# Kernel tuning notes

Hardware: AMD Instinct MI355X
Metric: run time of the kernel (lower is better)

Reference implementation:

```python
import jax, jax.numpy as jnp
import numpy as np

EPS = 1e-5


def _layer_norm(x, gamma, beta):
    mu = jnp.mean(x, axis=-1, keepdims=True)
    var = jnp.var(x, axis=-1, keepdims=True)
    return (x - mu) * jax.lax.rsqrt(var + EPS) * gamma + beta


def setup_inputs() -> dict:
    key = jax.random.key(0)
    B, I, H = 4096, 1024, 1024
    ks = jax.random.split(key, 6)
    x = jax.random.normal(ks[0], (B, I), dtype=jnp.float32)
    h = jax.random.normal(ks[1], (B, H), dtype=jnp.float32)
    c = jax.random.normal(ks[2], (B, H), dtype=jnp.float32)
    # nn.Linear(I+H, 4H): weight [4H, I+H], bias [4H]
    bound = 1.0 / np.sqrt(I + H)
    W = jax.random.uniform(ks[3], (4 * H, I + H), minval=-bound, maxval=bound, dtype=jnp.float32)
    b = jax.random.uniform(ks[4], (4 * H,), minval=-bound, maxval=bound, dtype=jnp.float32)
    inp = {"x": x, "h": h, "c": c, "W": W, "b": b}
    for name in ("i", "f", "g", "o", "c"):
        inp[f"ln_{name}_g"] = jnp.ones((H,), dtype=jnp.float32)
        inp[f"ln_{name}_b"] = jnp.zeros((H,), dtype=jnp.float32)
    return inp


def reference(x, h, c, W, b, ln_i_g, ln_i_b, ln_f_g, ln_f_b, ln_g_g, ln_g_b,
              ln_o_g, ln_o_b, ln_c_g, ln_c_b):
    H = h.shape[-1]
    xh = jnp.concatenate([x, h], axis=-1)              # [B, I+H]
    gates = xh @ W.T + b                               # [B, 4H]
    i_raw, f_raw, g_raw, o_raw = jnp.split(gates, 4, axis=-1)
    i = jax.nn.sigmoid(_layer_norm(i_raw, ln_i_g, ln_i_b))
    f = jax.nn.sigmoid(_layer_norm(f_raw, ln_f_g, ln_f_b))
    g = jnp.tanh(_layer_norm(g_raw, ln_g_g, ln_g_b))
    o = jax.nn.sigmoid(_layer_norm(o_raw, ln_o_g, ln_o_b))
    c_new = f * c + i * g
    h_new = o * jnp.tanh(_layer_norm(c_new, ln_c_g, ln_c_b))
    return (h_new, c_new)
```

## Files before the change

kernel.cpp:

```cpp
#include <hip/hip_runtime.h>
#include <hip/hip_bf16.h>

#define B_ROWS 4096
#define H_DIM  1024
#define K_DIM  2048
#define N_DIM  4096
#define NT32   64

typedef __attribute__((ext_vector_type(8))) short bf16x8;
typedef __attribute__((ext_vector_type(4))) float f32x4;

__device__ __forceinline__ unsigned short f2bf(float f) {
  union { float f; unsigned int u; } v; v.f = f;
  unsigned int u = v.u;
  return (unsigned short)((u + 0x7fffu + ((u >> 16) & 1u)) >> 16);
}
__device__ __forceinline__ float bf2f(unsigned short u) {
  union { unsigned int u; float f; } v; v.u = ((unsigned int)u) << 16;
  return v.f;
}

__device__ __forceinline__ void gload_lds16(const void* g, void* l) {
  __builtin_amdgcn_global_load_lds(
      (const __attribute__((address_space(1))) void*)g,
      (__attribute__((address_space(3))) void*)l, 16, 0, 0);
}

__global__ __launch_bounds__(256) void pack_kernel(
    const float* __restrict__ x, const float* __restrict__ h,
    const float* __restrict__ W, unsigned short* __restrict__ Abf,
    unsigned short* __restrict__ Wbf) {
  int bid = blockIdx.x;
  if (bid < 8192) {
    int t = bid * 256 + threadIdx.x;
    int e = t * 4;
    int row = e >> 11;
    int col = e & 2047;
    const float* src = (col < 1024) ? (x + (size_t)row * 1024 + col)
                                    : (h + (size_t)row * 1024 + (col - 1024));
    float4 v = *(const float4*)src;
    ushort4 o;
    o.x = f2bf(v.x); o.y = f2bf(v.y); o.z = f2bf(v.z); o.w = f2bf(v.w);
    *(ushort4*)(Abf + e) = o;
  } else {
    int t = (bid - 8192) * 256 + threadIdx.x;
    int e = t * 4;
    float4 v = *(const float4*)(W + e);
    ushort4 o;
    o.x = f2bf(v.x); o.y = f2bf(v.y); o.z = f2bf(v.z); o.w = f2bf(v.w);
    *(ushort4*)(Wbf + e) = o;
  }
}


#define UNR _Pragma("unroll")

#define TILE1(tt, BUF, FRa, FRb, FWa, FWb)                                   \
  {                                                                          \
    const int kt3 = ((tt) + 3) & (NT32 - 1);                                 \
    char* const Ld = lds + (((BUF) + 3) & 3) * 32768;                        \
    const unsigned short* pA = gAw + ((size_t)kt3 << 5);                     \
    const unsigned short* pB = gBw + ((size_t)kt3 << 5);                     \
    gload_lds16(pA, Ld + dstOfs);                                            \
    gload_lds16(pA + 16 * K_DIM, Ld + dstOfs + 1024);                        \
    gload_lds16(pB, Ld + 16384 + dstOfs);                                    \
    gload_lds16(pB + 16 * K_DIM, Ld + 16384 + dstOfs + 1024);                \
    asm volatile("s_waitcnt vmcnt(8)" ::: "memory");                         \
    __builtin_amdgcn_s_barrier();                                            \
    const char* const Ln = lds + (((BUF) + 1) & 3) * 32768;                  \
    UNR for (int mi = 0; mi < 8; ++mi)                                       \
      FWa[mi] = *(const bf16x8*)(Ln + (wm * 8 + mi) * 1024 + lofs);          \
    UNR for (int ni = 0; ni < 4; ++ni)                                       \
      FWb[ni] = *(const bf16x8*)(Ln + 16384 + (wn * 4 + ni) * 1024 + lofs);  \
    asm volatile("s_waitcnt lgkmcnt(12)" ::: "memory");                      \
    __builtin_amdgcn_sched_barrier(0);                                       \
    __builtin_amdgcn_s_setprio(1);                                           \
    UNR for (int mi = 0; mi < 8; ++mi)                                       \
      UNR for (int ni = 0; ni < 4; ++ni)                                     \
        acc[mi][ni] = __builtin_amdgcn_mfma_f32_16x16x32_bf16(               \
            FRa[mi], FRb[ni], acc[mi][ni], 0, 0, 0);                         \
    __builtin_amdgcn_s_setprio(0);                                           \
  }

#define PSTAGE(kt, BUFOFS)                                                   \
  {                                                                          \
    const unsigned short* pA = gAw + ((size_t)(kt) << 5);                    \
    const unsigned short* pB = gBw + ((size_t)(kt) << 5);                    \
    char* const Ld = lds + (BUFOFS);                                         \
    gload_lds16(pA, Ld + dstOfs);                                            \
    gload_lds16(pA + 16 * K_DIM, Ld + dstOfs + 1024);                        \
    gload_lds16(pB, Ld + 16384 + dstOfs);                                    \
    gload_lds16(pB + 16 * K_DIM, Ld + 16384 + dstOfs + 1024);                \
  }

__global__ __launch_bounds__(512, 2) void gemm_kernel(
    const unsigned short* __restrict__ A, const unsigned short* __restrict__ W,
    const float* __restrict__ bias, unsigned short* __restrict__ C) {
  __shared__ __align__(16) char lds[131072];

  const int tid = threadIdx.x;
  const int w = tid >> 6, l = tid & 63;
  const int wm = w >> 2, wn = w & 3;

  const int bid = blockIdx.x;
  const int xcd = bid & 7, li = bid >> 3;
  const int by = (xcd & 3) * 4 + (li >> 3);
  const int bx = ((xcd >> 2) << 3) + (li & 7);
  const int bm = by * 256, bn = bx * 256;

  const int lofs = (((l & 15) * 64) + ((l >> 4) * 16)) ^ ((l & 8) << 2);
  const int lane_r = (l >> 2) & 15;
  const int lane_c = ((l & 3) * 8) ^ (((l >> 5) & 1) * 16);

  const int dstOfs = w * 2048;
  const unsigned short* gAw = A + (size_t)(bm + 32 * w + lane_r) * K_DIM + lane_c;
  const unsigned short* gBw = W + (size_t)(bn + 32 * w + lane_r) * K_DIM + lane_c;

  f32x4 acc[8][4];
#pragma unroll
  for (int i = 0; i < 8; ++i)
#pragma unroll
    for (int j = 0; j < 4; ++j) acc[i][j] = (f32x4)0.0f;

  PSTAGE(0, 0);
  PSTAGE(1, 32768);
  PSTAGE(2, 65536);
  asm volatile("s_waitcnt vmcnt(8)" ::: "memory");
  __builtin_amdgcn_s_barrier();

  bf16x8 aP[8], bP[4], aQ[8], bQ[4];
#pragma unroll
  for (int mi = 0; mi < 8; ++mi)
    aP[mi] = *(const bf16x8*)(lds + (wm * 8 + mi) * 1024 + lofs);
#pragma unroll
  for (int ni = 0; ni < 4; ++ni)
    bP[ni] = *(const bf16x8*)(lds + 16384 + (wn * 4 + ni) * 1024 + lofs);

  for (int t = 0; t < NT32; t += 4) {
    TILE1(t + 0, 0, aP, bP, aQ, bQ);
    TILE1(t + 1, 1, aQ, bQ, aP, bP);
    TILE1(t + 2, 2, aP, bP, aQ, bQ);
    TILE1(t + 3, 3, aQ, bQ, aP, bP);
  }

  const int lm = l & 15, lq = l >> 4;
  float bv[4];
#pragma unroll
  for (int ni = 0; ni < 4; ++ni) bv[ni] = bias[bn + wn * 64 + ni * 16 + lm];
  unsigned short* Cb = C + (size_t)(bm + wm * 128) * N_DIM + bn + wn * 64;
#pragma unroll
  for (int mi = 0; mi < 8; ++mi)
#pragma unroll
    for (int j = 0; j < 4; ++j) {
      const size_t rofs = (size_t)(mi * 16 + lq * 4 + j) * N_DIM;
#pragma unroll
      for (int ni = 0; ni < 4; ++ni)
        Cb[rofs + ni * 16 + lm] = f2bf(acc[mi][ni][j] + bv[ni]);
    }
}

__device__ __forceinline__ float2 blk_sum2(float s, float q, float* red,
                                           int wid, int lane) {
#pragma unroll
  for (int o = 32; o >= 1; o >>= 1) {
    s += __shfl_xor(s, o, 64);
    q += __shfl_xor(q, o, 64);
  }
  __syncthreads();
  if (lane == 0) { red[wid * 2] = s; red[wid * 2 + 1] = q; }
  __syncthreads();
  s = red[0] + red[2] + red[4] + red[6];
  q = red[1] + red[3] + red[5] + red[7];
  return make_float2(s, q);
}

__device__ __forceinline__ float sigmoidf_(float x) {
  return 1.0f / (1.0f + __expf(-x));
}
__device__ __forceinline__ float tanhf_(float x) {
  return 1.0f - 2.0f / (__expf(2.0f * x) + 1.0f);
}

__global__ __launch_bounds__(256) void ln_lstm_kernel(
    const unsigned short* __restrict__ gates, const float* __restrict__ cprev,
    const float* __restrict__ g_i, const float* __restrict__ b_i,
    const float* __restrict__ g_f, const float* __restrict__ b_f,
    const float* __restrict__ g_g, const float* __restrict__ b_g,
    const float* __restrict__ g_o, const float* __restrict__ b_o,
    const float* __restrict__ g_c, const float* __restrict__ b_c,
    float* __restrict__ out) {
  const int b = blockIdx.x;
  const int t = threadIdx.x;
  const int wid = t >> 6, lane = t & 63;
  __shared__ float red[8];

  const unsigned short* grow = gates + (size_t)b * N_DIM;
  const int c0 = t * 4;

  float v[4][4];
#pragma unroll
  for (int g = 0; g < 4; g++) {
    ushort4 raw = *(const ushort4*)(grow + g * 1024 + c0);
    v[g][0] = bf2f(raw.x); v[g][1] = bf2f(raw.y);
    v[g][2] = bf2f(raw.z); v[g][3] = bf2f(raw.w);
  }

  const float4 gamma[4] = {*(const float4*)(g_i + c0), *(const float4*)(g_f + c0),
                           *(const float4*)(g_g + c0), *(const float4*)(g_o + c0)};
  const float4 beta[4]  = {*(const float4*)(b_i + c0), *(const float4*)(b_f + c0),
                           *(const float4*)(b_g + c0), *(const float4*)(b_o + c0)};

  float a[4][4];
#pragma unroll
  for (int g = 0; g < 4; g++) {
    float s = v[g][0] + v[g][1] + v[g][2] + v[g][3];
    float q = v[g][0]*v[g][0] + v[g][1]*v[g][1] + v[g][2]*v[g][2] + v[g][3]*v[g][3];
    float2 r = blk_sum2(s, q, red, wid, lane);
    float mu = r.x * (1.0f / 1024.0f);
    float var = r.y * (1.0f / 1024.0f) - mu * mu;
    float inv = rsqrtf(var + 1e-5f);
    const float* gm = (const float*)&gamma[g];
    const float* bt = (const float*)&beta[g];
#pragma unroll
    for (int j = 0; j < 4; j++) {
      float n = (v[g][j] - mu) * inv * gm[j] + bt[j];
      a[g][j] = (g == 2) ? tanhf_(n) : sigmoidf_(n);
    }
  }

  float4 cp = *(const float4*)(cprev + (size_t)b * 1024 + c0);
  const float* cpe = (const float*)&cp;
  float cn[4];
#pragma unroll
  for (int j = 0; j < 4; j++)
    cn[j] = a[1][j] * cpe[j] + a[0][j] * a[2][j];

  {
    float s = cn[0] + cn[1] + cn[2] + cn[3];
    float q = cn[0]*cn[0] + cn[1]*cn[1] + cn[2]*cn[2] + cn[3]*cn[3];
    float2 r = blk_sum2(s, q, red, wid, lane);
    float mu = r.x * (1.0f / 1024.0f);
    float var = r.y * (1.0f / 1024.0f) - mu * mu;
    float inv = rsqrtf(var + 1e-5f);
    float4 gm = *(const float4*)(g_c + c0);
    float4 bt = *(const float4*)(b_c + c0);
    const float* gme = (const float*)&gm;
    const float* bte = (const float*)&bt;
    float hn[4];
#pragma unroll
    for (int j = 0; j < 4; j++) {
      float n = (cn[j] - mu) * inv * gme[j] + bte[j];
      hn[j] = a[3][j] * tanhf_(n);
    }
    *(float4*)(out + (size_t)b * 1024 + c0) = make_float4(hn[0], hn[1], hn[2], hn[3]);
    *(float4*)(out + (size_t)B_ROWS * H_DIM + (size_t)b * 1024 + c0) =
        make_float4(cn[0], cn[1], cn[2], cn[3]);
  }
}

extern "C" void kernel_launch(void* const* d_in, const int* in_sizes, int n_in,
                              void* d_out, int out_size, void* d_ws,
                              size_t ws_size, hipStream_t stream) {
  const float* x    = (const float*)d_in[0];
  const float* h    = (const float*)d_in[1];
  const float* c    = (const float*)d_in[2];
  const float* W    = (const float*)d_in[3];
  const float* bias = (const float*)d_in[4];
  const float* ln_i_g = (const float*)d_in[5];
  const float* ln_i_b = (const float*)d_in[6];
  const float* ln_f_g = (const float*)d_in[7];
  const float* ln_f_b = (const float*)d_in[8];
  const float* ln_g_g = (const float*)d_in[9];
  const float* ln_g_b = (const float*)d_in[10];
  const float* ln_o_g = (const float*)d_in[11];
  const float* ln_o_b = (const float*)d_in[12];
  const float* ln_c_g = (const float*)d_in[13];
  const float* ln_c_b = (const float*)d_in[14];

  unsigned short* Abf = (unsigned short*)d_ws;
  unsigned short* Wbf = Abf + (size_t)B_ROWS * K_DIM;
  unsigned short* gates = Wbf + (size_t)N_DIM * K_DIM;

  pack_kernel<<<16384, 256, 0, stream>>>(x, h, W, Abf, Wbf);

  dim3 ggrid(256);
  gemm_kernel<<<ggrid, 512, 0, stream>>>(Abf, Wbf, bias, gates);

  ln_lstm_kernel<<<B_ROWS, 256, 0, stream>>>(
      gates, c, ln_i_g, ln_i_b, ln_f_g, ln_f_b, ln_g_g, ln_g_b,
      ln_o_g, ln_o_b, ln_c_g, ln_c_b, (float*)d_out);
}
```

Measured before the change: 105.3 us.

## Fuse fp32-to-bf16 conversion into GEMM mainloop, dropping the pack kernel

Removes the separate pack kernel that converted x, h and W to bf16 in a workspace. The GEMM now loads fp32 directly into registers, converts to bf16 and writes swizzled tiles into LDS. The pipeline changes from async global-to-LDS loads with a 3-deep prefetch to register-staged loads 2 tiles ahead, with full vmcnt and lgkmcnt waits and a barrier every tile. This saves the extra pack pass and its HBM round trip, but doubles the GEMM's global read bytes and adds conversion VALU work and serialization inside the mainloop.

After: 194.7 us. 85.0% more time.

```diff
diff --git a/kernel.cpp b/kernel.cpp
--- a/kernel.cpp
+++ b/kernel.cpp
@@ -20,82 +20,71 @@
   return v.f;
 }
 
-__device__ __forceinline__ void gload_lds16(const void* g, void* l) {
-  __builtin_amdgcn_global_load_lds(
-      (const __attribute__((address_space(1))) void*)g,
-      (__attribute__((address_space(3))) void*)l, 16, 0, 0);
-}
-
-__global__ __launch_bounds__(256) void pack_kernel(
-    const float* __restrict__ x, const float* __restrict__ h,
-    const float* __restrict__ W, unsigned short* __restrict__ Abf,
-    unsigned short* __restrict__ Wbf) {
-  int bid = blockIdx.x;
-  if (bid < 8192) {
-    int t = bid * 256 + threadIdx.x;
-    int e = t * 4;
-    int row = e >> 11;
-    int col = e & 2047;
-    const float* src = (col < 1024) ? (x + (size_t)row * 1024 + col)
-                                    : (h + (size_t)row * 1024 + (col - 1024));
-    float4 v = *(const float4*)src;
-    ushort4 o;
-    o.x = f2bf(v.x); o.y = f2bf(v.y); o.z = f2bf(v.z); o.w = f2bf(v.w);
-    *(ushort4*)(Abf + e) = o;
-  } else {
-    int t = (bid - 8192) * 256 + threadIdx.x;
-    int e = t * 4;
-    float4 v = *(const float4*)(W + e);
-    ushort4 o;
-    o.x = f2bf(v.x); o.y = f2bf(v.y); o.z = f2bf(v.z); o.w = f2bf(v.w);
-    *(ushort4*)(Wbf + e) = o;
-  }
-}
-
 
 #define UNR _Pragma("unroll")
 
-#define TILE1(tt, BUF, FRa, FRb, FWa, FWb)                                   \
-  {                                                                          \
-    const int kt3 = ((tt) + 3) & (NT32 - 1);                                 \
-    char* const Ld = lds + (((BUF) + 3) & 3) * 32768;                        \
-    const unsigned short* pA = gAw + ((size_t)kt3 << 5);                     \
-    const unsigned short* pB = gBw + ((size_t)kt3 << 5);                     \
-    gload_lds16(pA, Ld + dstOfs);                                            \
-    gload_lds16(pA + 16 * K_DIM, Ld + dstOfs + 1024);                        \
-    gload_lds16(pB, Ld + 16384 + dstOfs);                                    \
-    gload_lds16(pB + 16 * K_DIM, Ld + 16384 + dstOfs + 1024);                \
-    asm volatile("s_waitcnt vmcnt(8)" ::: "memory");                         \
-    __builtin_amdgcn_s_barrier();                                            \
-    const char* const Ln = lds + (((BUF) + 1) & 3) * 32768;                  \
+#define ISSUE_LOADS(kt)                                                      \
+  {                                                                          \
+    const int kk = (kt);                                                     \
+    const float* a0 = (kk < 32) ? (pAx0 + kk * 32) : (pAh0 + (kk - 32) * 32);\
+    const float* a1 = (kk < 32) ? (pAx1 + kk * 32) : (pAh1 + (kk - 32) * 32);\
+    LA00 = *(const float4*)(a0);                                             \
+    LA01 = *(const float4*)(a0 + 4);                                         \
+    LA10 = *(const float4*)(a1);                                             \
+    LA11 = *(const float4*)(a1 + 4);                                         \
+    LB00 = *(const float4*)(pB0 + kk * 32);                                  \
+    LB01 = *(const float4*)(pB0 + kk * 32 + 4);                              \
+    LB10 = *(const float4*)(pB1 + kk * 32);                                  \
+    LB11 = *(const float4*)(pB1 + kk * 32 + 4);                              \
+  }
+
+#define PK8(dst, v0, v1)                                                     \
+  {                                                                          \
+    bf16x8 pk;                                                               \
+    pk[0] = (short)f2bf(v0.x); pk[1] = (short)f2bf(v0.y);                    \
+    pk[2] = (short)f2bf(v0.z); pk[3] = (short)f2bf(v0.w);                    \
+    pk[4] = (short)f2bf(v1.x); pk[5] = (short)f2bf(v1.y);                    \
+    pk[6] = (short)f2bf(v1.z); pk[7] = (short)f2bf(v1.w);                    \
+    *(bf16x8*)(dst) = pk;                                                    \
+  }
+
+#define CVT_WRITE(BUFOFS)                                                    \
+  {                                                                          \
+    char* const Lw = lds + (BUFOFS);                                         \
+    PK8(Lw + (2 * w + 0) * 1024 + wofs, LA00, LA01);                         \
+    PK8(Lw + (2 * w + 1) * 1024 + wofs, LA10, LA11);                         \
+    PK8(Lw + 16384 + (2 * w + 0) * 1024 + wofs, LB00, LB01);                 \
+    PK8(Lw + 16384 + (2 * w + 1) * 1024 + wofs, LB10, LB11);                 \
+  }
+
+#define TILE1(tt, BUF)                                                       \
+  {                                                                          \
+    asm volatile("s_waitcnt vmcnt(0)" ::: "memory");                         \
+    __builtin_amdgcn_sched_barrier(0);                                       \
+    CVT_WRITE((((BUF) + 1) & 3) * 32768);                                    \
+    __builtin_amdgcn_sched_barrier(0);                                       \
+    ISSUE_LOADS(((tt) + 2) & (NT32 - 1));                                    \
+    const char* const Lc = lds + (BUF) * 32768;                              \
+    bf16x8 aF[8], bF[4];                                                     \
     UNR for (int mi = 0; mi < 8; ++mi)                                       \
-      FWa[mi] = *(const bf16x8*)(Ln + (wm * 8 + mi) * 1024 + lofs);          \
+      aF[mi] = *(const bf16x8*)(Lc + (wm * 8 + mi) * 1024 + lofs);           \
     UNR for (int ni = 0; ni < 4; ++ni)                                       \
-      FWb[ni] = *(const bf16x8*)(Ln + 16384 + (wn * 4 + ni) * 1024 + lofs);  \
-    asm volatile("s_waitcnt lgkmcnt(12)" ::: "memory");                      \
+      bF[ni] = *(const bf16x8*)(Lc + 16384 + (wn * 4 + ni) * 1024 + lofs);   \
+    asm volatile("s_waitcnt lgkmcnt(0)" ::: "memory");                       \
     __builtin_amdgcn_sched_barrier(0);                                       \
     __builtin_amdgcn_s_setprio(1);                                           \
     UNR for (int mi = 0; mi < 8; ++mi)                                       \
       UNR for (int ni = 0; ni < 4; ++ni)                                     \
         acc[mi][ni] = __builtin_amdgcn_mfma_f32_16x16x32_bf16(               \
-            FRa[mi], FRb[ni], acc[mi][ni], 0, 0, 0);                         \
+            aF[mi], bF[ni], acc[mi][ni], 0, 0, 0);                           \
     __builtin_amdgcn_s_setprio(0);                                           \
-  }
-
-#define PSTAGE(kt, BUFOFS)                                                   \
-  {                                                                          \
-    const unsigned short* pA = gAw + ((size_t)(kt) << 5);                    \
-    const unsigned short* pB = gBw + ((size_t)(kt) << 5);                    \
-    char* const Ld = lds + (BUFOFS);                                         \
-    gload_lds16(pA, Ld + dstOfs);                                            \
-    gload_lds16(pA + 16 * K_DIM, Ld + dstOfs + 1024);                        \
-    gload_lds16(pB, Ld + 16384 + dstOfs);                                    \
-    gload_lds16(pB + 16 * K_DIM, Ld + 16384 + dstOfs + 1024);                \
+    __builtin_amdgcn_s_barrier();                                            \
   }
 
 __global__ __launch_bounds__(512, 2) void gemm_kernel(
-    const unsigned short* __restrict__ A, const unsigned short* __restrict__ W,
-    const float* __restrict__ bias, unsigned short* __restrict__ C) {
+    const float* __restrict__ x, const float* __restrict__ h,
+    const float* __restrict__ W, const float* __restrict__ bias,
+    unsigned short* __restrict__ C) {
   __shared__ __align__(16) char lds[131072];
 
   const int tid = threadIdx.x;
@@ -109,12 +98,18 @@
   const int bm = by * 256, bn = bx * 256;
 
   const int lofs = (((l & 15) * 64) + ((l >> 4) * 16)) ^ ((l & 8) << 2);
-  const int lane_r = (l >> 2) & 15;
-  const int lane_c = ((l & 3) * 8) ^ (((l >> 5) & 1) * 16);
-
-  const int dstOfs = w * 2048;
-  const unsigned short* gAw = A + (size_t)(bm + 32 * w + lane_r) * K_DIM + lane_c;
-  const unsigned short* gBw = W + (size_t)(bn + 32 * w + lane_r) * K_DIM + lane_c;
+  const int wofs = (l * 16) ^ (l & 32);
+
+  const int srow = l >> 2, scol = (l & 3) * 8;
+  const int ar0 = bm + 32 * w + srow, ar1 = ar0 + 16;
+  const float* pAx0 = x + (size_t)ar0 * 1024 + scol;
+  const float* pAx1 = x + (size_t)ar1 * 1024 + scol;
+  const float* pAh0 = h + (size_t)ar0 * 1024 + scol;
+  const float* pAh1 = h + (size_t)ar1 * 1024 + scol;
+  const float* pB0 = W + (size_t)(bn + 32 * w + srow) * K_DIM + scol;
+  const float* pB1 = W + (size_t)(bn + 32 * w + 16 + srow) * K_DIM + scol;
+
+  float4 LA00, LA01, LA10, LA11, LB00, LB01, LB10, LB11;
 
   f32x4 acc[8][4];
 #pragma unroll
@@ -122,25 +117,20 @@
 #pragma unroll
     for (int j = 0; j < 4; ++j) acc[i][j] = (f32x4)0.0f;
 
-  PSTAGE(0, 0);
-  PSTAGE(1, 32768);
-  PSTAGE(2, 65536);
-  asm volatile("s_waitcnt vmcnt(8)" ::: "memory");
+  ISSUE_LOADS(0);
+  asm volatile("s_waitcnt vmcnt(0)" ::: "memory");
+  __builtin_amdgcn_sched_barrier(0);
+  CVT_WRITE(0);
+  __builtin_amdgcn_sched_barrier(0);
+  ISSUE_LOADS(1);
+  asm volatile("s_waitcnt lgkmcnt(0)" ::: "memory");
   __builtin_amdgcn_s_barrier();
 
-  bf16x8 aP[8], bP[4], aQ[8], bQ[4];
-#pragma unroll
-  for (int mi = 0; mi < 8; ++mi)
-    aP[mi] = *(const bf16x8*)(lds + (wm * 8 + mi) * 1024 + lofs);
-#pragma unroll
-  for (int ni = 0; ni < 4; ++ni)
-    bP[ni] = *(const bf16x8*)(lds + 16384 + (wn * 4 + ni) * 1024 + lofs);
-
   for (int t = 0; t < NT32; t += 4) {
-    TILE1(t + 0, 0, aP, bP, aQ, bQ);
-    TILE1(t + 1, 1, aQ, bQ, aP, bP);
-    TILE1(t + 2, 2, aP, bP, aQ, bQ);
-    TILE1(t + 3, 3, aQ, bQ, aP, bP);
+    TILE1(t + 0, 0);
+    TILE1(t + 1, 1);
+    TILE1(t + 2, 2);
+    TILE1(t + 3, 3);
   }
 
   const int lm = l & 15, lq = l >> 4;
@@ -277,14 +267,10 @@
   const float* ln_c_g = (const float*)d_in[13];
   const float* ln_c_b = (const float*)d_in[14];
 
-  unsigned short* Abf = (unsigned short*)d_ws;
-  unsigned short* Wbf = Abf + (size_t)B_ROWS * K_DIM;
-  unsigned short* gates = Wbf + (size_t)N_DIM * K_DIM;
-
-  pack_kernel<<<16384, 256, 0, stream>>>(x, h, W, Abf, Wbf);
+  unsigned short* gates = (unsigned short*)d_ws;
 
   dim3 ggrid(256);
-  gemm_kernel<<<ggrid, 512, 0, stream>>>(Abf, Wbf, bias, gates);
+  gemm_kernel<<<ggrid, 512, 0, stream>>>(x, h, W, bias, gates);
 
   ln_lstm_kernel<<<B_ROWS, 256, 0, stream>>>(
       gates, c, ln_i_g, ln_i_b, ln_f_g, ln_f_b, ln_g_g, ln_g_b,
```
